# Performance work log

Hardware: AMD Instinct MI355X
Metric: run time of the kernel (lower is better)

The kernel has to match this reference:

```python
import jax, jax.numpy as jnp
import numpy as np

N_QUBITS = 4
DIM = 16  # 2**N_QUBITS
BATCH = 2_097_152


def _pauli_sign_tables():
    # Wire 0 is the most-significant bit in pennylane default.qubit ordering.
    bits = (np.arange(DIM)[:, None] >> np.arange(N_QUBITS - 1, -1, -1)[None, :]) & 1
    z_signs = (1 - 2 * bits).astype(np.float32)  # [16, 4], <Z_i> signs per basis state
    pairs = [(i, j) for i in range(N_QUBITS) for j in range(i + 1, N_QUBITS)]
    zz_signs = np.stack([z_signs[:, i] * z_signs[:, j] for i, j in pairs], axis=1)  # [16, 6]
    return jnp.asarray(z_signs), jnp.asarray(zz_signs)

Z_SIGNS, ZZ_SIGNS = _pauli_sign_tables()


def setup_inputs() -> dict:
    key = jax.random.key(0)
    ks = jax.random.split(key, 6)
    return {
        "x": jax.random.normal(ks[0], (BATCH, DIM), jnp.float32),
        "u_weights": jax.random.normal(ks[1], (N_QUBITS, 2), jnp.float32),
        "w1": jax.random.normal(ks[2], (16, 10), jnp.float32) * 0.3,
        "b1": jnp.zeros((16,), jnp.float32),
        "w2": jax.random.normal(ks[3], (2, 16), jnp.float32) * 0.25,
        "b2": jnp.zeros((2,), jnp.float32),
    }


def _circuit_features(x, u_weights):
    # StatePrep with normalize=True
    state = x / jnp.linalg.norm(x, axis=1, keepdims=True)
    state = state.astype(jnp.complex64).reshape(-1, 2, 2, 2, 2)  # [B, q0, q1, q2, q3]
    half_th = 0.5 * u_weights[:, 0]
    half_ph = 0.5 * u_weights[:, 1]
    c, s = jnp.cos(half_th), jnp.sin(half_th)
    for q in range(N_QUBITS):
        ry = jnp.stack([jnp.stack([c[q], -s[q]]),
                        jnp.stack([s[q], c[q]])]).astype(jnp.complex64)
        e = jnp.exp(-1j * half_ph[q].astype(jnp.complex64))
        rz = jnp.diag(jnp.stack([e, jnp.conj(e)]))
        u = rz @ ry  # RZ(phi) after RY(theta), single fused 2x2 gate
        state = jnp.moveaxis(state, q + 1, -1)
        state = state @ u.T  # new[a] = sum_b u[a,b] * old[b]
        state = jnp.moveaxis(state, -1, q + 1)
    probs = jnp.abs(state.reshape(-1, DIM)) ** 2  # [B, 16]
    z = probs @ Z_SIGNS    # [B, 4]  <Z_i>
    zz = probs @ ZZ_SIGNS  # [B, 6]  <Z_i Z_j>, i<j
    return jnp.concatenate([z, zz], axis=1)  # [B, 10]


def reference(x, u_weights, w1, b1, w2, b2):
    feats = _circuit_features(x, u_weights)
    h = jax.nn.relu(feats @ w1.T + b1)
    return h @ w2.T + b2  # [B, 2]
```

## Files before the change

kernel.cpp:

```cpp
#include <hip/hip_runtime.h>
#include <math.h>


__global__ void qc_prep(const float* __restrict__ uw, const float* __restrict__ w1,
                        const float* __restrict__ b1, const float* __restrict__ w2,
                        const float* __restrict__ b2, float* __restrict__ P) {
    int t = threadIdx.x;
    if (t < 4) {
        float th = 0.5f * uw[t * 2 + 0];
        P[t]     = cosf(th);
        P[4 + t] = sinf(th);
    }
    int k = t >> 4, j = t & 15;
    float z0 = 1.0f - 2.0f * ((k >> 3) & 1);
    float z1 = 1.0f - 2.0f * ((k >> 2) & 1);
    float z2 = 1.0f - 2.0f * ((k >> 1) & 1);
    float z3 = 1.0f - 2.0f * ((k >> 0) & 1);
    float S[10] = { z0, z1, z2, z3,
                    z0 * z1, z0 * z2, z0 * z3, z1 * z2, z1 * z3, z2 * z3 };
    float acc = 0.0f;
#pragma unroll
    for (int f = 0; f < 10; ++f) acc += w1[j * 10 + f] * S[f];
    P[8 + k * 16 + j] = acc;

    if (t < 16) P[264 + t] = b1[t];
    if (t < 32) P[280 + t] = w2[t];
    if (t < 2)  P[312 + t] = b2[t];
}

__global__ __launch_bounds__(256) void qc_main(const float* __restrict__ x,
                                               const float* __restrict__ P,
                                               float* __restrict__ out, int batch) {
    int s = blockIdx.x * blockDim.x + threadIdx.x;
    if (s >= batch) return;

    const float4* xv = (const float4*)(x + (size_t)s * 16);
    float4 a0 = xv[0], a1 = xv[1], a2 = xv[2], a3 = xv[3];

    float y[16] = { a0.x, a0.y, a0.z, a0.w,
                    a1.x, a1.y, a1.z, a1.w,
                    a2.x, a2.y, a2.z, a2.w,
                    a3.x, a3.y, a3.z, a3.w };

    float ss = 0.0f;
#pragma unroll
    for (int i = 0; i < 16; ++i) ss = fmaf(y[i], y[i], ss);
    float r = 1.0f / ss;

#pragma unroll
    for (int q = 0; q < 4; ++q) {
        const float cq = P[q], sq = P[4 + q];
        const int st = 8 >> q;
#pragma unroll
        for (int i = 0; i < 16; ++i) {
            if ((i & st) == 0) {
                float a = y[i], b = y[i + st];
                y[i]      = cq * a - sq * b;
                y[i + st] = fmaf(sq, a, cq * b);
            }
        }
    }

    float p[16];
#pragma unroll
    for (int i = 0; i < 16; ++i) p[i] = y[i] * y[i];

    float tacc[16];
#pragma unroll
    for (int j = 0; j < 16; ++j) tacc[j] = 0.0f;
#pragma unroll
    for (int k = 0; k < 16; ++k) {
        float pk = p[k];
        const float* Ak = P + 8 + k * 16;
#pragma unroll
        for (int j = 0; j < 16; ++j) tacc[j] = fmaf(Ak[j], pk, tacc[j]);
    }

    float o0 = P[312], o1 = P[313];
#pragma unroll
    for (int j = 0; j < 16; ++j) {
        float h = fmaf(tacc[j], r, P[264 + j]);
        h = fmaxf(h, 0.0f);
        o0 = fmaf(P[280 + j], h, o0);
        o1 = fmaf(P[296 + j], h, o1);
    }

    ((float2*)out)[s] = make_float2(o0, o1);
}

extern "C" void kernel_launch(void* const* d_in, const int* in_sizes, int n_in,
                              void* d_out, int out_size, void* d_ws, size_t ws_size,
                              hipStream_t stream) {
    const float* x  = (const float*)d_in[0];
    const float* uw = (const float*)d_in[1];
    const float* w1 = (const float*)d_in[2];
    const float* b1 = (const float*)d_in[3];
    const float* w2 = (const float*)d_in[4];
    const float* b2 = (const float*)d_in[5];
    float* out = (float*)d_out;
    float* P   = (float*)d_ws;

    int batch = in_sizes[0] / 16;

    hipLaunchKernelGGL(qc_prep, dim3(1), dim3(256), 0, stream, uw, w1, b1, w2, b2, P);
    int blocks = (batch + 255) / 256;
    hipLaunchKernelGGL(qc_main, dim3(blocks), dim3(256), 0, stream, x, P, out, batch);
}
```

Baseline: 204.6 us.

## Fuse prep into main kernel, stage x via LDS coalesced loads, use Walsh-Hadamard features

Drops the separate prep launch: each block now computes its own rotation cos/sin and stages w1, b1, w2 and b2 in shared memory. Input rows are loaded cooperatively as coalesced float4 reads into a padded shared tile, and each thread then reads its own row from there. The 16x16 probability-to-hidden matmul is replaced by an in-register Walsh-Hadamard transform that yields the Z and ZZ expectations, followed by a 10x16 matmul against transposed w1. In exchange, every block repeats the tiny setup work, uses about 20KB of shared memory and adds a block barrier.

```diff
diff --git a/kernel.cpp b/kernel.cpp
--- a/kernel.cpp
+++ b/kernel.cpp
@@ -2,61 +2,69 @@
 #include <math.h>
 
 
-__global__ void qc_prep(const float* __restrict__ uw, const float* __restrict__ w1,
-                        const float* __restrict__ b1, const float* __restrict__ w2,
-                        const float* __restrict__ b2, float* __restrict__ P) {
-    int t = threadIdx.x;
+#define PAD 20
+
+__global__ __launch_bounds__(256) void qc_fused(
+    const float* __restrict__ x, const float* __restrict__ uw,
+    const float* __restrict__ w1, const float* __restrict__ b1,
+    const float* __restrict__ w2, const float* __restrict__ b2,
+    float* __restrict__ out, int batch)
+{
+    __shared__ float sX[256 * PAD];
+    __shared__ float sW1t[160];
+    __shared__ float sB1[16];
+    __shared__ float sW2[32];
+    __shared__ float sB2[2];
+    __shared__ float sCS[8];
+
+    const int t = threadIdx.x;
+
     if (t < 4) {
-        float th = 0.5f * uw[t * 2 + 0];
-        P[t]     = cosf(th);
-        P[4 + t] = sinf(th);
+        float th = 0.5f * uw[2 * t];
+        sCS[t]     = cosf(th);
+        sCS[4 + t] = sinf(th);
     }
-    int k = t >> 4, j = t & 15;
-    float z0 = 1.0f - 2.0f * ((k >> 3) & 1);
-    float z1 = 1.0f - 2.0f * ((k >> 2) & 1);
-    float z2 = 1.0f - 2.0f * ((k >> 1) & 1);
-    float z3 = 1.0f - 2.0f * ((k >> 0) & 1);
-    float S[10] = { z0, z1, z2, z3,
-                    z0 * z1, z0 * z2, z0 * z3, z1 * z2, z1 * z3, z2 * z3 };
-    float acc = 0.0f;
+    if (t < 160) sW1t[t] = w1[(t & 15) * 10 + (t >> 4)];
+    if (t < 16)  sB1[t] = b1[t];
+    if (t < 32)  sW2[t] = w2[t];
+    if (t < 2)   sB2[t] = b2[t];
+
+    const float4* xv4 = (const float4*)x;
+    const long nv4 = (long)batch * 4;
+    const long base4 = (long)blockIdx.x * 1024;
 #pragma unroll
-    for (int f = 0; f < 10; ++f) acc += w1[j * 10 + f] * S[f];
-    P[8 + k * 16 + j] = acc;
+    for (int r2 = 0; r2 < 4; ++r2) {
+        int f = t + 256 * r2;
+        long g = base4 + f;
+        float4 v = (g < nv4) ? xv4[g] : make_float4(0.f, 0.f, 0.f, 0.f);
+        ((float4*)(sX + (f >> 2) * PAD))[f & 3] = v;
+    }
+    __syncthreads();
 
-    if (t < 16) P[264 + t] = b1[t];
-    if (t < 32) P[280 + t] = w2[t];
-    if (t < 2)  P[312 + t] = b2[t];
-}
+    const float* myx = sX + t * PAD;
+    float y[16];
+#pragma unroll
+    for (int i = 0; i < 4; ++i) {
+        float4 v = ((const float4*)myx)[i];
+        y[4 * i + 0] = v.x; y[4 * i + 1] = v.y;
+        y[4 * i + 2] = v.z; y[4 * i + 3] = v.w;
+    }
 
-__global__ __launch_bounds__(256) void qc_main(const float* __restrict__ x,
-                                               const float* __restrict__ P,
-                                               float* __restrict__ out, int batch) {
-    int s = blockIdx.x * blockDim.x + threadIdx.x;
-    if (s >= batch) return;
-
-    const float4* xv = (const float4*)(x + (size_t)s * 16);
-    float4 a0 = xv[0], a1 = xv[1], a2 = xv[2], a3 = xv[3];
-
-    float y[16] = { a0.x, a0.y, a0.z, a0.w,
-                    a1.x, a1.y, a1.z, a1.w,
-                    a2.x, a2.y, a2.z, a2.w,
-                    a3.x, a3.y, a3.z, a3.w };
-
-    float ss = 0.0f;
+    float ss = 0.f;
 #pragma unroll
     for (int i = 0; i < 16; ++i) ss = fmaf(y[i], y[i], ss);
-    float r = 1.0f / ss;
+    const float rn = 1.0f / ss;
 
 #pragma unroll
     for (int q = 0; q < 4; ++q) {
-        const float cq = P[q], sq = P[4 + q];
+        const float cq = sCS[q], sq = sCS[4 + q];
         const int st = 8 >> q;
 #pragma unroll
         for (int i = 0; i < 16; ++i) {
             if ((i & st) == 0) {
                 float a = y[i], b = y[i + st];
-                y[i]      = cq * a - sq * b;
-                y[i + st] = fmaf(sq, a, cq * b);
+                y[i]      = fmaf(cq, a, -sq * b);
+                y[i + st] = fmaf(sq, a,  cq * b);
             }
         }
     }
@@ -64,28 +72,42 @@
     float p[16];
 #pragma unroll
     for (int i = 0; i < 16; ++i) p[i] = y[i] * y[i];
+#pragma unroll
+    for (int st = 1; st < 16; st <<= 1) {
+#pragma unroll
+        for (int i = 0; i < 16; ++i) {
+            if ((i & st) == 0) {
+                float a = p[i], b = p[i + st];
+                p[i]      = a + b;
+                p[i + st] = a - b;
+            }
+        }
+    }
+
+    constexpr int bmap[10] = {8, 4, 2, 1, 12, 10, 9, 6, 5, 3};
 
     float tacc[16];
 #pragma unroll
-    for (int j = 0; j < 16; ++j) tacc[j] = 0.0f;
+    for (int j = 0; j < 16; ++j) tacc[j] = 0.f;
 #pragma unroll
-    for (int k = 0; k < 16; ++k) {
-        float pk = p[k];
-        const float* Ak = P + 8 + k * 16;
+    for (int f = 0; f < 10; ++f) {
+        const float ff = p[bmap[f]];
+        const float* col = sW1t + f * 16;
 #pragma unroll
-        for (int j = 0; j < 16; ++j) tacc[j] = fmaf(Ak[j], pk, tacc[j]);
+        for (int j = 0; j < 16; ++j) tacc[j] = fmaf(col[j], ff, tacc[j]);
     }
 
-    float o0 = P[312], o1 = P[313];
+    float o0 = sB2[0], o1 = sB2[1];
 #pragma unroll
     for (int j = 0; j < 16; ++j) {
-        float h = fmaf(tacc[j], r, P[264 + j]);
-        h = fmaxf(h, 0.0f);
-        o0 = fmaf(P[280 + j], h, o0);
-        o1 = fmaf(P[296 + j], h, o1);
+        float h = fmaf(tacc[j], rn, sB1[j]);
+        h = fmaxf(h, 0.f);
+        o0 = fmaf(sW2[j],      h, o0);
+        o1 = fmaf(sW2[16 + j], h, o1);
     }
 
-    ((float2*)out)[s] = make_float2(o0, o1);
+    const long sidx = (long)blockIdx.x * 256 + t;
+    if (sidx < batch) ((float2*)out)[sidx] = make_float2(o0, o1);
 }
 
 extern "C" void kernel_launch(void* const* d_in, const int* in_sizes, int n_in,
@@ -98,11 +120,9 @@
     const float* w2 = (const float*)d_in[4];
     const float* b2 = (const float*)d_in[5];
     float* out = (float*)d_out;
-    float* P   = (float*)d_ws;
 
     int batch = in_sizes[0] / 16;
-
-    hipLaunchKernelGGL(qc_prep, dim3(1), dim3(256), 0, stream, uw, w1, b1, w2, b2, P);
     int blocks = (batch + 255) / 256;
-    hipLaunchKernelGGL(qc_main, dim3(blocks), dim3(256), 0, stream, x, P, out, batch);
+    hipLaunchKernelGGL(qc_fused, dim3(blocks), dim3(256), 0, stream,
+                       x, uw, w1, b1, w2, b2, out, batch);
 }
```

Measured after the change: 208.8 us. 1.02x slower.
